# Optimization experiments

Hardware: AMD Instinct MI355X
Metric: run time of the kernel (lower is better)

Reference implementation:

```python
import jax, jax.numpy as jnp
import numpy as np
from jax import lax

WINDOW_SIZE = 11
SIGMA = 1.5
MAX_VAL = 1.0
C1 = (0.01 * MAX_VAL) ** 2
C2 = (0.03 * MAX_VAL) ** 2
PAD = (WINDOW_SIZE - 1) // 2


def _gaussian_kernel2d(ksize: int, sigma: float) -> jnp.ndarray:
    x = jnp.arange(ksize, dtype=jnp.float32) - ksize // 2
    g = jnp.exp(-(x ** 2) / (2.0 * sigma ** 2))
    g = g / jnp.sum(g)
    return jnp.outer(g, g)  # [k, k]


def _filter2d(x: jnp.ndarray, kernel2d: jnp.ndarray) -> jnp.ndarray:
    # depthwise conv: x [B,C,H,W], kernel repeated per channel -> [C,1,k,k]
    c = x.shape[1]
    k = jnp.broadcast_to(kernel2d[None, None], (c, 1, WINDOW_SIZE, WINDOW_SIZE)).astype(x.dtype)
    return lax.conv_general_dilated(
        x, k,
        window_strides=(1, 1),
        padding=((PAD, PAD), (PAD, PAD)),
        dimension_numbers=("NCHW", "OIHW", "NCHW"),
        feature_group_count=c,
    )


def setup_inputs() -> dict:
    key = jax.random.key(0)
    k1, k2 = jax.random.split(key)
    img1 = jax.random.uniform(k1, (16, 3, 512, 512), dtype=jnp.float32)
    img2 = jax.random.uniform(k2, (16, 3, 512, 512), dtype=jnp.float32)
    return {"img1": img1, "img2": img2}


def reference(img1, img2):
    kernel = _gaussian_kernel2d(WINDOW_SIZE, SIGMA)
    mu1 = _filter2d(img1, kernel)
    mu2 = _filter2d(img2, kernel)
    mu1_sq = mu1 * mu1
    mu2_sq = mu2 * mu2
    mu1_mu2 = mu1 * mu2
    sigma1_sq = _filter2d(img1 * img1, kernel) - mu1_sq
    sigma2_sq = _filter2d(img2 * img2, kernel) - mu2_sq
    sigma12 = _filter2d(img1 * img2, kernel) - mu1_mu2
    ssim_map = ((2.0 * mu1_mu2 + C1) * (2.0 * sigma12 + C2)) / (
        (mu1_sq + mu2_sq + C1) * (sigma1_sq + sigma2_sq + C2)
    )
    loss = jnp.clip(1.0 - ssim_map, 0.0, 1.0) / 2.0
    return jnp.mean(loss)  # reduction='mean'
```

## Files before the change

### kernel.cpp

```cpp
#include <hip/hip_runtime.h>


#define BATCH  16
#define CHAN   3
#define H_     512
#define W_     512
#define HW     (H_ * W_)
#define CH_H   64
#define NPIX   ((long)BATCH*CHAN*H_*W_)

#define GW0 0.0010284f
#define GW1 0.0075988f
#define GW2 0.0360008f
#define GW3 0.1093554f
#define GW4 0.2130056f
#define GW5 0.2660117f

typedef float v2 __attribute__((ext_vector_type(2)));

__device__ __forceinline__ float wg(int k) {
    return (k == 0 || k == 10) ? GW0
         : (k == 1 || k == 9)  ? GW1
         : (k == 2 || k == 8)  ? GW2
         : (k == 3 || k == 7)  ? GW3
         : (k == 4 || k == 6)  ? GW4 : GW5;
}

__device__ __forceinline__ v2 pfma(v2 a, v2 b, v2 c) {
#if __has_builtin(__builtin_elementwise_fma)
    return __builtin_elementwise_fma(a, b, c);
#else
    v2 r; r.x = fmaf(a.x, b.x, c.x); r.y = fmaf(a.y, b.y, c.y); return r;
#endif
}
__device__ __forceinline__ v2 psfma(float s, v2 b, v2 c) {
    v2 sv; sv.x = s; sv.y = s;
    return pfma(sv, b, c);
}

__device__ __forceinline__ float ssim_retire(float mu1, float mu2,
                                             float x11, float x22, float x12) {
    const float c1 = 1.0e-4f;
    const float c2 = 9.0e-4f;
    float mu1s = mu1 * mu1;
    float mu2s = mu2 * mu2;
    float m12  = mu1 * mu2;
    float num  = (2.0f * m12 + c1) * (2.0f * (x12 - m12) + c2);
    float den  = (mu1s + mu2s + c1) * ((x11 - mu1s) + (x22 - mu2s) + c2);
#if __has_builtin(__builtin_amdgcn_rcpf)
    float l = 1.0f - num * __builtin_amdgcn_rcpf(den);
#else
    float l = 1.0f - num / den;
#endif
    return fminf(fmaxf(l, 0.0f), 1.0f);
}

#define DECL(i) v2 P##i = {0.f, 0.f}, Q##i = {0.f, 0.f}; float E##i = 0.f
#define ACCI(i) do { const float wj_ = wg(10 - (i));             \
    P##i = psfma(wj_, hmm, P##i);                                \
    Q##i = psfma(wj_, hss, Q##i);                                \
    E##i = fmaf(wj_, hm12, E##i); } while (0)
#define SHIFT(i, j) P##i = P##j; Q##i = Q##j; E##i = E##j

__global__ __launch_bounds__(256, 3) void ssim_kernel(const float* __restrict__ img1,
                                                      const float* __restrict__ img2,
                                                      float* __restrict__ out) {
    __shared__ __align__(16) v2 sp[4][80];
    __shared__ float wsum[4];

    const int tid  = threadIdx.x;
    const int lane = tid & 63;
    const int wv   = tid >> 6;

    const int wid   = blockIdx.x * 4 + wv;
    const int plane = wid >> 6;
    const int rem   = wid & 63;
    const int strip = rem & 7;
    const int chunk = rem >> 3;
    const int y0 = chunk * CH_H;
    const int c0 = strip * 64;

    const int  colg  = c0 - 5 + lane;
    const bool colOk = (colg >= 0);
    const int  colC  = colOk ? colg : 0;
    const int  colg2  = c0 + 59 + lane;
    const bool colOk2 = (lane < 11) && (colg2 < W_);
    const int  col2C  = colOk2 ? colg2 : 0;

    const size_t pb = (size_t)plane * HW;
    const float* __restrict__ p1  = img1 + pb + colC;
    const float* __restrict__ p2  = img2 + pb + colC;
    const float* __restrict__ p1b = img1 + pb + col2C;
    const float* __restrict__ p2b = img2 + pb + col2C;

    v2* st = sp[wv];

    DECL(0); DECL(1); DECL(2); DECL(3); DECL(4); DECL(5);
    DECL(6); DECL(7); DECL(8); DECL(9); DECL(10);
    float lsum = 0.0f;

    float cv1, cv2, cv1b, cv2b;
    {
        int r = y0 - 5;
        bool rok = (unsigned)r < (unsigned)H_;
        size_t off = (size_t)(rok ? r : 0) * W_;
        cv1  = (rok && colOk)  ? p1[off]  : 0.0f;
        cv2  = (rok && colOk)  ? p2[off]  : 0.0f;
        cv1b = (rok && colOk2) ? p1b[off] : 0.0f;
        cv2b = (rok && colOk2) ? p2b[off] : 0.0f;
    }

#pragma unroll 2
    for (int step = 0; step < 74; ++step) {
        const int yy = step - 10;

        {
            v2 v; v.x = cv1; v.y = cv2;
            st[lane] = v;
            if (lane < 11) { v2 vb; vb.x = cv1b; vb.y = cv2b; st[64 + lane] = vb; }
        }
        __asm__ __volatile__("" ::: "memory");

        {
            int r = y0 + yy + 6;
            bool rok = (unsigned)r < (unsigned)H_;
            size_t off = (size_t)(rok ? r : 0) * W_;
            cv1  = (rok && colOk)  ? p1[off]  : 0.0f;
            cv2  = (rok && colOk)  ? p2[off]  : 0.0f;
            cv1b = (rok && colOk2) ? p1b[off] : 0.0f;
            cv2b = (rok && colOk2) ? p2b[off] : 0.0f;
        }

        v2 hmm = {0.f, 0.f}, hss = {0.f, 0.f};
        float hm12 = 0.f;
#pragma unroll
        for (int k = 0; k < 11; ++k) {
            v2 ab = st[lane + k];
            float wk = wg(k);
            v2 t = ab;
            t.x *= wk; t.y *= wk;
            hmm += t;
            hss = pfma(t, ab, hss);
            hm12 = fmaf(t.x, ab.y, hm12);
        }
        __asm__ __volatile__("" ::: "memory");

        ACCI(0); ACCI(1); ACCI(2); ACCI(3); ACCI(4); ACCI(5);
        ACCI(6); ACCI(7); ACCI(8); ACCI(9); ACCI(10);

        if (yy >= 0) lsum += ssim_retire(P0.x, P0.y, Q0.x, Q0.y, E0);

        SHIFT(0, 1); SHIFT(1, 2); SHIFT(2, 3); SHIFT(3, 4); SHIFT(4, 5);
        SHIFT(5, 6); SHIFT(6, 7); SHIFT(7, 8); SHIFT(8, 9); SHIFT(9, 10);
        P10 = (v2){0.f, 0.f}; Q10 = (v2){0.f, 0.f}; E10 = 0.f;
    }

#pragma unroll
    for (int off = 32; off > 0; off >>= 1) lsum += __shfl_down(lsum, off);
    if (lane == 0) wsum[wv] = lsum;
    __syncthreads();
    if (tid == 0) {
        float bs = wsum[0] + wsum[1] + wsum[2] + wsum[3];
        atomicAdd(out, bs * (0.5f / (float)NPIX));
    }
}

extern "C" void kernel_launch(void* const* d_in, const int* in_sizes, int n_in,
                              void* d_out, int out_size, void* d_ws, size_t ws_size,
                              hipStream_t stream) {
    const float* img1 = (const float*)d_in[0];
    const float* img2 = (const float*)d_in[1];
    float* out = (float*)d_out;

    hipMemsetAsync(out, 0, sizeof(float), stream);

    ssim_kernel<<<dim3(8 * 8 * BATCH * CHAN / 4), 256, 0, stream>>>(img1, img2, out);
}
```

Before: 153.3 us.

## Replace LDS row staging with per-lane vector loads of 12-wide windows

Drops the shared-memory row buffer used for the horizontal pass. Each lane now loads its own 12-float window per image with three 16-byte vector loads per row. Edge columns are handled by clamping the window start and shifting the per-lane Gaussian weights, and out-of-range rows are zeroed with a multiplier. This removes LDS writes and reads and the halo-lane branch, but each row is loaded about 12 times from cache instead of once. It also raises register pressure, since six vec4 buffers and twelve weights are held per lane and the occupancy hint in launch bounds is removed. Loads at offset bcc are not 16-byte aligned, which may split accesses.

```diff
diff --git a/kernel.cpp b/kernel.cpp
--- a/kernel.cpp
+++ b/kernel.cpp
@@ -7,6 +7,7 @@
 #define W_     512
 #define HW     (H_ * W_)
 #define CH_H   64
+#define NSTEP  (CH_H + 10)
 #define NPIX   ((long)BATCH*CHAN*H_*W_)
 
 #define GW0 0.0010284f
@@ -16,15 +17,8 @@
 #define GW4 0.2130056f
 #define GW5 0.2660117f
 
-typedef float v2 __attribute__((ext_vector_type(2)));
-
-__device__ __forceinline__ float wg(int k) {
-    return (k == 0 || k == 10) ? GW0
-         : (k == 1 || k == 9)  ? GW1
-         : (k == 2 || k == 8)  ? GW2
-         : (k == 3 || k == 7)  ? GW3
-         : (k == 4 || k == 6)  ? GW4 : GW5;
-}
+typedef float v2  __attribute__((ext_vector_type(2)));
+typedef float v4f __attribute__((ext_vector_type(4)));
 
 __device__ __forceinline__ v2 pfma(v2 a, v2 b, v2 c) {
 #if __has_builtin(__builtin_elementwise_fma)
@@ -36,6 +30,14 @@
 __device__ __forceinline__ v2 psfma(float s, v2 b, v2 c) {
     v2 sv; sv.x = s; sv.y = s;
     return pfma(sv, b, c);
+}
+
+__device__ __forceinline__ float wgk(int k) {
+    return (k == 0 || k == 10) ? GW0
+         : (k == 1 || k == 9)  ? GW1
+         : (k == 2 || k == 8)  ? GW2
+         : (k == 3 || k == 7)  ? GW3
+         : (k == 4 || k == 6)  ? GW4 : GW5;
 }
 
 __device__ __forceinline__ float ssim_retire(float mu1, float mu2,
@@ -56,16 +58,18 @@
 }
 
 #define DECL(i) v2 P##i = {0.f, 0.f}, Q##i = {0.f, 0.f}; float E##i = 0.f
-#define ACCI(i) do { const float wj_ = wg(10 - (i));             \
+#define ACCI(i) do { const float wj_ = wgk(10 - (i));            \
     P##i = psfma(wj_, hmm, P##i);                                \
     Q##i = psfma(wj_, hss, Q##i);                                \
-    E##i = fmaf(wj_, hm12, E##i); } while (0)
+    E##i = fmaf(wj_, hmx, E##i); } while (0)
 #define SHIFT(i, j) P##i = P##j; Q##i = Q##j; E##i = E##j
 
-__global__ __launch_bounds__(256, 3) void ssim_kernel(const float* __restrict__ img1,
-                                                      const float* __restrict__ img2,
-                                                      float* __restrict__ out) {
-    __shared__ __align__(16) v2 sp[4][80];
+#define EL(a_, b_, c_, j_) ((j_) < 4 ? (a_)[(j_) & 3]                 \
+                          : (j_) < 8 ? (b_)[(j_) & 3] : (c_)[(j_) & 3])
+
+__global__ __launch_bounds__(256) void ssim_kernel(const float* __restrict__ img1,
+                                                   const float* __restrict__ img2,
+                                                   float* __restrict__ out) {
     __shared__ float wsum[4];
 
     const int tid  = threadIdx.x;
@@ -80,70 +84,81 @@
     const int y0 = chunk * CH_H;
     const int c0 = strip * 64;
 
-    const int  colg  = c0 - 5 + lane;
-    const bool colOk = (colg >= 0);
-    const int  colC  = colOk ? colg : 0;
-    const int  colg2  = c0 + 59 + lane;
-    const bool colOk2 = (lane < 11) && (colg2 < W_);
-    const int  col2C  = colOk2 ? colg2 : 0;
+    const int bc  = c0 + lane - 5;
+    const int bcc = min(max(bc, 0), W_ - 12);
+    const int s   = bcc - bc;
+    float wgm[12];
+#pragma unroll
+    for (int j = 0; j < 12; ++j) {
+        int ki = j + s;
+        float w = 0.0f;
+        w = (ki == 0 || ki == 10) ? GW0 : w;
+        w = (ki == 1 || ki == 9)  ? GW1 : w;
+        w = (ki == 2 || ki == 8)  ? GW2 : w;
+        w = (ki == 3 || ki == 7)  ? GW3 : w;
+        w = (ki == 4 || ki == 6)  ? GW4 : w;
+        w = (ki == 5)             ? GW5 : w;
+        wgm[j] = w;
+    }
 
     const size_t pb = (size_t)plane * HW;
-    const float* __restrict__ p1  = img1 + pb + colC;
-    const float* __restrict__ p2  = img2 + pb + colC;
-    const float* __restrict__ p1b = img1 + pb + col2C;
-    const float* __restrict__ p2b = img2 + pb + col2C;
-
-    v2* st = sp[wv];
+    const float* __restrict__ p1 = img1 + pb + bcc;
+    const float* __restrict__ p2 = img2 + pb + bcc;
 
     DECL(0); DECL(1); DECL(2); DECL(3); DECL(4); DECL(5);
     DECL(6); DECL(7); DECL(8); DECL(9); DECL(10);
     float lsum = 0.0f;
 
-    float cv1, cv2, cv1b, cv2b;
+    v4f a0, a1, a2, b0, b1, b2;
+    float rmC;
     {
         int r = y0 - 5;
-        bool rok = (unsigned)r < (unsigned)H_;
-        size_t off = (size_t)(rok ? r : 0) * W_;
-        cv1  = (rok && colOk)  ? p1[off]  : 0.0f;
-        cv2  = (rok && colOk)  ? p2[off]  : 0.0f;
-        cv1b = (rok && colOk2) ? p1b[off] : 0.0f;
-        cv2b = (rok && colOk2) ? p2b[off] : 0.0f;
+        rmC = ((unsigned)r < (unsigned)H_) ? 1.0f : 0.0f;
+        size_t off = (size_t)((unsigned)r < (unsigned)H_ ? r : 0) << 9;
+        a0 = *(const v4f*)(p1 + off);
+        a1 = *(const v4f*)(p1 + off + 4);
+        a2 = *(const v4f*)(p1 + off + 8);
+        b0 = *(const v4f*)(p2 + off);
+        b1 = *(const v4f*)(p2 + off + 4);
+        b2 = *(const v4f*)(p2 + off + 8);
     }
 
 #pragma unroll 2
-    for (int step = 0; step < 74; ++step) {
+    for (int step = 0; step < NSTEP; ++step) {
         const int yy = step - 10;
 
+        v4f na0, na1, na2, nb0, nb1, nb2;
+        float rmN;
         {
-            v2 v; v.x = cv1; v.y = cv2;
-            st[lane] = v;
-            if (lane < 11) { v2 vb; vb.x = cv1b; vb.y = cv2b; st[64 + lane] = vb; }
-        }
-        __asm__ __volatile__("" ::: "memory");
-
-        {
-            int r = y0 + yy + 6;
+            int r = y0 + step - 4;
             bool rok = (unsigned)r < (unsigned)H_;
-            size_t off = (size_t)(rok ? r : 0) * W_;
-            cv1  = (rok && colOk)  ? p1[off]  : 0.0f;
-            cv2  = (rok && colOk)  ? p2[off]  : 0.0f;
-            cv1b = (rok && colOk2) ? p1b[off] : 0.0f;
-            cv2b = (rok && colOk2) ? p2b[off] : 0.0f;
+            rmN = rok ? 1.0f : 0.0f;
+            size_t off = (size_t)(rok ? r : 0) << 9;
+            na0 = *(const v4f*)(p1 + off);
+            na1 = *(const v4f*)(p1 + off + 4);
+            na2 = *(const v4f*)(p1 + off + 8);
+            nb0 = *(const v4f*)(p2 + off);
+            nb1 = *(const v4f*)(p2 + off + 4);
+            nb2 = *(const v4f*)(p2 + off + 8);
         }
 
-        v2 hmm = {0.f, 0.f}, hss = {0.f, 0.f};
-        float hm12 = 0.f;
+        float hm1 = 0.f, hm2 = 0.f, hm11 = 0.f, hm22 = 0.f, hm12v = 0.f;
 #pragma unroll
-        for (int k = 0; k < 11; ++k) {
-            v2 ab = st[lane + k];
-            float wk = wg(k);
-            v2 t = ab;
-            t.x *= wk; t.y *= wk;
-            hmm += t;
-            hss = pfma(t, ab, hss);
-            hm12 = fmaf(t.x, ab.y, hm12);
+        for (int j = 0; j < 12; ++j) {
+            float av = EL(a0, a1, a2, j);
+            float bv = EL(b0, b1, b2, j);
+            float wv_ = wgm[j];
+            float ta = wv_ * av;
+            float tb = wv_ * bv;
+            hm1 += ta;
+            hm2 += tb;
+            hm11 = fmaf(ta, av, hm11);
+            hm22 = fmaf(tb, bv, hm22);
+            hm12v = fmaf(ta, bv, hm12v);
         }
-        __asm__ __volatile__("" ::: "memory");
+        v2 hmm = {hm1 * rmC, hm2 * rmC};
+        v2 hss = {hm11 * rmC, hm22 * rmC};
+        float hmx = hm12v * rmC;
 
         ACCI(0); ACCI(1); ACCI(2); ACCI(3); ACCI(4); ACCI(5);
         ACCI(6); ACCI(7); ACCI(8); ACCI(9); ACCI(10);
@@ -153,6 +168,10 @@
         SHIFT(0, 1); SHIFT(1, 2); SHIFT(2, 3); SHIFT(3, 4); SHIFT(4, 5);
         SHIFT(5, 6); SHIFT(6, 7); SHIFT(7, 8); SHIFT(8, 9); SHIFT(9, 10);
         P10 = (v2){0.f, 0.f}; Q10 = (v2){0.f, 0.f}; E10 = 0.f;
+
+        a0 = na0; a1 = na1; a2 = na2;
+        b0 = nb0; b1 = nb1; b2 = nb2;
+        rmC = rmN;
     }
 
 #pragma unroll
```

Measured after the change: 158.1 us. 3.2% more time.
